# Kernel tuning notes

Measured on AMD Instinct MI355X. Metric: run time of the kernel, lower is better.

The kernel has to match this reference:

```python
import jax, jax.numpy as jnp
import numpy as np
import math

N, S, R = 1, 128, 256
CM, CZ, C, MSA_H, PAIR_H, CTM, FF = 256, 128, 32, 8, 4, 128, 4
SCALE = 1.0 / math.sqrt(C)


def _ln(x, w, b):
    m = jnp.mean(x, -1, keepdims=True)
    v = jnp.var(x, -1, keepdims=True)
    return (x - m) / jnp.sqrt(v + 1e-5) * w + b


def _gated_attn(x, gate_w, qkv_w, out_w, head, bias=None):
    # x: [n, s, r, cin]; attention over r within each (n, s, head)
    n, s, r, _ = x.shape
    gate = jax.nn.sigmoid(x @ gate_w).reshape(n, s, r, head, C)
    qkv = (x @ qkv_w).reshape(n, s, r, 3, head, C)
    q, k, v = qkv[..., 0, :, :], qkv[..., 1, :, :], qkv[..., 2, :, :]
    sim = jax.nn.softmax(jnp.einsum('nsqhc,nskhc->nshqk', q, k) * SCALE, axis=-1)
    if bias is not None:
        sim = sim + bias  # NOTE: source adds bias AFTER softmax; kept faithful
    att = jnp.einsum('nshqk,nskhc->nsqhc', sim, v) * gate
    return att.reshape(n, s, r, head * C) @ out_w


def _tri_mul(x, n1w, n1b, n2w, n2b, p1, p2, p3, p4, p5, p6, incoming):
    xn = _ln(x, n1w, n1b)
    a = jax.nn.sigmoid(xn @ p1) * (xn @ p2)
    b = jax.nn.sigmoid(xn @ p3) * (xn @ p4)
    if incoming:
        p = jnp.einsum('nrsk,nrtk->nstk', a, b)
        g = jnp.swapaxes(jax.nn.sigmoid(xn @ p6), 1, 2)
    else:
        p = jnp.einsum('nsrk,ntrk->nstk', a, b)
        g = jax.nn.sigmoid(xn @ p6)
    return (_ln(p, n2w, n2b) @ p5) * g


def setup_inputs() -> dict:
    keys = iter(jax.random.split(jax.random.key(0), 80))

    def rn(shape, scale=0.02):
        return jax.random.normal(next(keys), shape, dtype=jnp.float32) * scale

    ones = lambda n: jnp.ones((n,), jnp.float32)
    zeros = lambda n: jnp.zeros((n,), jnp.float32)
    d = dict(
        msa_repr=rn((N, S, R, CM), 1.0),
        pair_repr=rn((N, R, R, CZ), 1.0),
        row_norm_m_w=ones(CM), row_norm_m_b=zeros(CM),
        row_norm_z_w=ones(CZ), row_norm_z_b=zeros(CZ),
        row_gate=rn((CM, MSA_H * C)), row_qkv=rn((CM, 3 * MSA_H * C)),
        row_out=rn((MSA_H * C, CM)), row_bias=rn((CZ, MSA_H)),
        col_norm_w=ones(CM), col_norm_b=zeros(CM),
        col_gate=rn((CM, MSA_H * C)), col_qkv=rn((CM, 3 * MSA_H * C)),
        col_out=rn((MSA_H * C, CM)),
        mt_norm_w=ones(CM), mt_norm_b=zeros(CM),
        mt_p1=rn((CM, FF * CM)), mt_p2=rn((FF * CM, CM)),
        outer_norm_w=ones(CM), outer_norm_b=zeros(CM),
        outer_p1=rn((CM, C)), outer_p2=rn((CM, C)), outer_out=rn((C * C, CZ)),
        tmo_n1_w=ones(CZ), tmo_n1_b=zeros(CZ), tmo_n2_w=ones(CTM), tmo_n2_b=zeros(CTM),
        tmo_p1=rn((CZ, CTM)), tmo_p2=rn((CZ, CTM)), tmo_p3=rn((CZ, CTM)), tmo_p4=rn((CZ, CTM)),
        tmo_p5=rn((CTM, CZ)), tmo_p6=rn((CZ, CZ)),
        tmi_n1_w=ones(CZ), tmi_n1_b=zeros(CZ), tmi_n2_w=ones(CTM), tmi_n2_b=zeros(CTM),
        tmi_p1=rn((CZ, CTM)), tmi_p2=rn((CZ, CTM)), tmi_p3=rn((CZ, CTM)), tmi_p4=rn((CZ, CTM)),
        tmi_p5=rn((CTM, CZ)), tmi_p6=rn((CZ, CZ)),
        tas_norm_w=ones(CZ), tas_norm_b=zeros(CZ),
        tas_gate=rn((CZ, PAIR_H * C)), tas_qkv=rn((CZ, 3 * PAIR_H * C)),
        tas_out=rn((PAIR_H * C, CZ)), tas_bias=rn((CZ, PAIR_H)),
        tae_norm_w=ones(CZ), tae_norm_b=zeros(CZ),
        tae_gate=rn((CZ, PAIR_H * C)), tae_qkv=rn((CZ, 3 * PAIR_H * C)),
        tae_out=rn((PAIR_H * C, CZ)), tae_bias=rn((CZ, PAIR_H)),
        pt_norm_w=ones(CZ), pt_norm_b=zeros(CZ),
        pt_p1=rn((CZ, FF * CZ)), pt_p2=rn((FF * CZ, CZ)),
    )
    return d


def reference(msa_repr, pair_repr, row_norm_m_w, row_norm_m_b, row_norm_z_w, row_norm_z_b, row_gate, row_qkv, row_out, row_bias, col_norm_w, col_norm_b, col_gate, col_qkv, col_out, mt_norm_w, mt_norm_b, mt_p1, mt_p2, outer_norm_w, outer_norm_b, outer_p1, outer_p2, outer_out, tmo_n1_w, tmo_n1_b, tmo_n2_w, tmo_n2_b, tmo_p1, tmo_p2, tmo_p3, tmo_p4, tmo_p5, tmo_p6, tmi_n1_w, tmi_n1_b, tmi_n2_w, tmi_n2_b, tmi_p1, tmi_p2, tmi_p3, tmi_p4, tmi_p5, tmi_p6, tas_norm_w, tas_norm_b, tas_gate, tas_qkv, tas_out, tas_bias, tae_norm_w, tae_norm_b, tae_gate, tae_qkv, tae_out, tae_bias, pt_norm_w, pt_norm_b, pt_p1, pt_p2):
    msa, pair = msa_repr, pair_repr
    # 1. MSA row attention with pair bias
    xm = _ln(msa, row_norm_m_w, row_norm_m_b)
    xz = _ln(pair, row_norm_z_w, row_norm_z_b)
    bias = jnp.transpose(xz @ row_bias, (0, 3, 1, 2))[:, None]  # [N,1,H,R,R]
    msa = msa + _gated_attn(xm, row_gate, row_qkv, row_out, MSA_H, bias)
    # 2. MSA column attention
    xm = _ln(msa, col_norm_w, col_norm_b)
    msa = msa + jnp.swapaxes(_gated_attn(jnp.swapaxes(xm, 1, 2), col_gate, col_qkv, col_out, MSA_H), 1, 2)
    # 3. MSA transition
    xm = _ln(msa, mt_norm_w, mt_norm_b)
    msa = msa + jax.nn.relu(xm @ mt_p1) @ mt_p2
    # 4. outer product mean (no division in source; sum over s)
    xm = _ln(msa, outer_norm_w, outer_norm_b)
    a = jnp.swapaxes(xm @ outer_p1, 1, 2)  # [n,r,s,c]
    b = jnp.swapaxes(xm @ outer_p2, 1, 2)  # [n,t,s,c]
    outer = jnp.einsum('nrsc,ntse->nrtce', a, b).reshape(a.shape[0], a.shape[1], b.shape[1], C * C)
    pair = pair + outer @ outer_out
    # 5/6. triangle multiplicative updates (outgoing then incoming)
    pair = pair + _tri_mul(pair, tmo_n1_w, tmo_n1_b, tmo_n2_w, tmo_n2_b, tmo_p1, tmo_p2, tmo_p3, tmo_p4, tmo_p5, tmo_p6, False)
    pair = pair + _tri_mul(pair, tmi_n1_w, tmi_n1_b, tmi_n2_w, tmi_n2_b, tmi_p1, tmi_p2, tmi_p3, tmi_p4, tmi_p5, tmi_p6, True)
    # 7. triangle attention (node start)
    xz = _ln(pair, tas_norm_w, tas_norm_b)
    bias = jnp.transpose(xz @ tas_bias, (0, 1, 3, 2))[:, :, :, None, :]  # [N,S,H,1,R]
    pair = pair + _gated_attn(xz, tas_gate, tas_qkv, tas_out, PAIR_H, bias)
    # 8. triangle attention (node end): transpose residue axes
    xz = jnp.swapaxes(_ln(pair, tae_norm_w, tae_norm_b), 1, 2)
    bias = jnp.transpose(xz @ tae_bias, (0, 1, 3, 2))[:, :, :, None, :]
    pair = pair + jnp.swapaxes(_gated_attn(xz, tae_gate, tae_qkv, tae_out, PAIR_H, bias), 1, 2)
    # 9. pair transition
    xz = _ln(pair, pt_norm_w, pt_norm_b)
    pair = pair + jax.nn.relu(xz @ pt_p1) @ pt_p2
    return msa, pair
```

## Files before the change

kernel.cpp:

```cpp
#include <hip/hip_runtime.h>
#include <hip/hip_bf16.h>
#include <stdint.h>

typedef __hip_bfloat16 bf16;
typedef __attribute__((ext_vector_type(4))) int   i32x4;
typedef __attribute__((ext_vector_type(4))) float f32x4;


__device__ __forceinline__ float toF(float x){ return x; }
__device__ __forceinline__ float toF(bf16 x){ return __bfloat162float(x); }
__device__ __forceinline__ bf16  toB(float x){ return __float2bfloat16(x); }

__device__ __forceinline__ void gload16(const bf16* g, bf16* l){
    __builtin_amdgcn_global_load_lds((const __attribute__((address_space(1))) void*)g,
                                     (__attribute__((address_space(3))) void*)l, 16, 0, 0);
}

__global__ void cvt_w_k(const void* __restrict__ in, bf16* __restrict__ out, int n,
                        const uint32_t* __restrict__ probe){
    bool isbf = (probe[0] == 0x3F803F80u);
    int i = blockIdx.x*256 + threadIdx.x;
    if (i < n) out[i] = isbf ? ((const bf16*)in)[i] : toB(((const float*)in)[i]);
}
__global__ void cvt_wT_k(const void* __restrict__ in, bf16* __restrict__ out, int K, int N,
                         const uint32_t* __restrict__ probe){
    bool isbf = (probe[0] == 0x3F803F80u);
    int i = blockIdx.x*256 + threadIdx.x;
    if (i < K*N){
        float v = isbf ? toF(((const bf16*)in)[i]) : ((const float*)in)[i];
        int k = i / N, n = i - k*N;
        out[(size_t)n*K + k] = toB(v);
    }
}
__global__ void in2f_k(const void* __restrict__ in, float* __restrict__ out, int n,
                       const uint32_t* __restrict__ probe){
    bool isbf = (probe[0] == 0x3F803F80u);
    int i = blockIdx.x*256 + threadIdx.x;
    if (i < n) out[i] = isbf ? toF(((const bf16*)in)[i]) : ((const float*)in)[i];
}

template<typename T>
__global__ void ln_k(const T* __restrict__ x, const bf16* __restrict__ w, const bf16* __restrict__ b,
                     bf16* __restrict__ out, int D){
    int row = blockIdx.x, c = threadIdx.x;
    float v = toF(x[(size_t)row*D + c]);
    float s1 = v, s2 = v*v;
    #pragma unroll
    for (int o=32;o>0;o>>=1){ s1 += __shfl_down(s1,o); s2 += __shfl_down(s2,o); }
    __shared__ float r1[4], r2[4];
    int lane = c & 63, wid = c >> 6;
    if (lane==0){ r1[wid]=s1; r2[wid]=s2; }
    __syncthreads();
    int nw = blockDim.x >> 6;
    float m=0.f, q=0.f;
    for (int i=0;i<nw;i++){ m+=r1[i]; q+=r2[i]; }
    m /= (float)D; q = q/(float)D - m*m;
    float inv = rsqrtf(q + 1e-5f);
    out[(size_t)row*D + c] = toB((v-m)*inv*toF(w[c]) + toF(b[c]));
}

template<int MODE, int HN>
__global__ __launch_bounds__(256) void bproj_k(const bf16* __restrict__ xz, const bf16* __restrict__ Wb,
                                               float* __restrict__ outb){
    __shared__ float WbS[128*HN];
    const int i = blockIdx.x, t = threadIdx.x;
    for (int idx = t; idx < 128*HN; idx += 256) WbS[idx] = toF(Wb[idx]);
    __syncthreads();
    const bf16* row = xz + ((size_t)i*256 + t)*128;
    float d[HN] = {};
    #pragma unroll 4
    for (int c8 = 0; c8 < 16; ++c8){
        uint4 v = *(const uint4*)(row + c8*8);
        bf16 tmp[8]; *(uint4*)tmp = v;
        #pragma unroll
        for (int u=0;u<8;u++){
            float x = toF(tmp[u]);
            #pragma unroll
            for (int h=0;h<HN;h++) d[h] += x * WbS[(c8*8+u)*HN + h];
        }
    }
    #pragma unroll
    for (int h=0;h<HN;h++){
        size_t idx = (MODE==0) ? ((size_t)h*65536 + (size_t)i*256 + t)
                   : (MODE==1) ? ((size_t)(i*HN+h)*256 + t)
                               : ((size_t)(t*HN+h)*256 + i);
        outb[idx] = d[h];
    }
}

template<int ACT, int MUL, int RES>
__global__ __launch_bounds__(256) void mgemm_k(const bf16* __restrict__ A, const bf16* __restrict__ Bt,
                                               bf16* __restrict__ C, float* __restrict__ Res,
                                               const bf16* __restrict__ Mul,
                                               int M, int N, int K, int ldbt, int res_off, int gtrans){
    __shared__ alignas(16) bf16 As[128*32];
    __shared__ alignas(16) bf16 Bs[128*32];
    const int tid  = threadIdx.x;
    const int m0   = blockIdx.y << 7, n0 = blockIdx.x << 7;
    const int lane = tid & 63, w = tid >> 6;
    const int wr   = (w >> 1) << 6, wc = (w & 1) << 6;
    const int fr   = lane & 15, fq = lane >> 4;
    const int sr = tid >> 2, sc = (tid & 3) << 3;
    const bf16* ga = A  + (size_t)(m0 + sr)*K    + sc;
    const bf16* gb = Bt + (size_t)(n0 + sr)*ldbt + sc;
    bf16* la = As + tid*8;
    bf16* lb = Bs + tid*8;
    const size_t gaS = (size_t)64*K, gbS = (size_t)64*ldbt;

    f32x4 acc[4][4] = {};
    for (int k0=0; k0<K; k0+=32){
        gload16(ga, la);        gload16(ga + gaS, la + 2048);
        gload16(gb, lb);        gload16(gb + gbS, lb + 2048);
        ga += 32; gb += 32;
        __syncthreads();
        i32x4 af[4], bv[4];
        #pragma unroll
        for (int i=0;i<4;i++) af[i] = *(const i32x4*)(As + ((wr + i*16 + fr) << 5) + (fq << 3));
        #pragma unroll
        for (int j=0;j<4;j++) bv[j] = *(const i32x4*)(Bs + ((wc + j*16 + fr) << 5) + (fq << 3));
        #pragma unroll
        for (int i=0;i<4;i++)
            #pragma unroll
            for (int j=0;j<4;j++)
                asm("v_mfma_f32_16x16x32_bf16 %0, %1, %2, %0"
                    : "+v"(acc[i][j]) : "v"(af[i]), "v"(bv[j]));
        __syncthreads();
    }
    #pragma unroll
    for (int i=0;i<4;i++){
        const int mB = m0 + wr + i*16 + (fq << 2);
        #pragma unroll
        for (int j=0;j<4;j++){
            const int n = n0 + wc + j*16 + fr;
            #pragma unroll
            for (int r=0;r<4;r++){
                int m = mB + r;
                float x = acc[i][j][r];
                if (ACT==1) x = 1.f/(1.f + __expf(-x));
                else if (ACT==2) x = fmaxf(x, 0.f);
                if (MUL){
                    int mr = gtrans ? (((m & 255) << 8) | (m >> 8)) : m;
                    x *= toF(Mul[(size_t)mr*N + n]);
                }
                if (RES) Res[(size_t)(m + res_off)*N + n] += x;
                else     C[(size_t)m*N + n] = toB(x);
            }
        }
    }
}

__global__ __launch_bounds__(256) void btrimul_k(const bf16* __restrict__ aT, const bf16* __restrict__ bT,
                                                 bf16* __restrict__ pT){
    __shared__ alignas(16) bf16 As[128*32];
    __shared__ alignas(16) bf16 Bs[128*32];
    const int tid  = threadIdx.x;
    const int m0   = blockIdx.y << 7, n0 = blockIdx.x << 7;
    const size_t zb = (size_t)blockIdx.z << 16;
    const int lane = tid & 63, w = tid >> 6;
    const int wr   = (w >> 1) << 6, wc = (w & 1) << 6;
    const int fr   = lane & 15, fq = lane >> 4;
    const int sr = tid >> 2, sc = (tid & 3) << 3;
    const bf16* ga = aT + zb + (size_t)(m0 + sr)*256 + sc;
    const bf16* gb = bT + zb + (size_t)(n0 + sr)*256 + sc;
    bf16* la = As + tid*8;
    bf16* lb = Bs + tid*8;
    const size_t gS = (size_t)64*256;

    f32x4 acc[4][4] = {};
    for (int k0=0; k0<256; k0+=32){
        gload16(ga, la);        gload16(ga + gS, la + 2048);
        gload16(gb, lb);        gload16(gb + gS, lb + 2048);
        ga += 32; gb += 32;
        __syncthreads();
        i32x4 af[4], bv[4];
        #pragma unroll
        for (int i=0;i<4;i++) af[i] = *(const i32x4*)(As + ((wr + i*16 + fr) << 5) + (fq << 3));
        #pragma unroll
        for (int j=0;j<4;j++) bv[j] = *(const i32x4*)(Bs + ((wc + j*16 + fr) << 5) + (fq << 3));
        #pragma unroll
        for (int i=0;i<4;i++)
            #pragma unroll
            for (int j=0;j<4;j++)
                asm("v_mfma_f32_16x16x32_bf16 %0, %1, %2, %0"
                    : "+v"(acc[i][j]) : "v"(af[i]), "v"(bv[j]));
        __syncthreads();
    }
    #pragma unroll
    for (int i=0;i<4;i++){
        const int mB = m0 + wr + i*16 + (fq << 2);
        #pragma unroll
        for (int j=0;j<4;j++){
            const int n = n0 + wc + j*16 + fr;
            #pragma unroll
            for (int r=0;r<4;r++)
                pT[zb + (size_t)(mB + r)*256 + n] = toB(acc[i][j][r]);
        }
    }
}

__global__ __launch_bounds__(256) void rc2k_k(const bf16* __restrict__ in, bf16* __restrict__ out, int swap){
    __shared__ uint16_t T[128][137];
    const int tt = blockIdx.x, tid = threadIdx.x;
    size_t base_pp, out_off; int ppstride;
    if (!swap){ base_pp = (size_t)tt*128;                  ppstride = 1;   out_off = (size_t)tt*128; }
    else      { int J = tt>>1, I0 = (tt&1)*128;
                base_pp = (size_t)I0*256 + J;              ppstride = 256; out_off = (size_t)J*256 + I0; }
    for (int it=0; it<8; ++it){
        int idx = tid + it*256;
        int r = idx >> 4, c8 = (idx & 15) << 3;
        uint4 v = *(const uint4*)(in + (base_pp + (size_t)r*ppstride)*128 + c8);
        uint16_t tmp[8]; *(uint4*)tmp = v;
        #pragma unroll
        for (int t=0;t<8;t++) T[r][c8+t] = tmp[t];
    }
    __syncthreads();
    for (int it=0; it<8; ++it){
        int idx = tid + it*256;
        int k = idx >> 4, r8 = (idx & 15) << 3;
        uint16_t tmp[8];
        #pragma unroll
        for (int t=0;t<8;t++) tmp[t] = T[r8+t][k];
        *(uint4*)(out + (size_t)k*65536 + out_off + r8) = *(uint4*)tmp;
    }
}
__global__ __launch_bounds__(256) void k2rc_k(const bf16* __restrict__ in, bf16* __restrict__ out){
    __shared__ uint16_t T[128][137];
    const int tt = blockIdx.x, tid = threadIdx.x;
    const size_t a0 = (size_t)tt*128;
    for (int it=0; it<8; ++it){
        int idx = tid + it*256;
        int k = idx >> 4, r8 = (idx & 15) << 3;
        uint4 v = *(const uint4*)(in + (size_t)k*65536 + a0 + r8);
        uint16_t tmp[8]; *(uint4*)tmp = v;
        #pragma unroll
        for (int t=0;t<8;t++) T[r8+t][k] = tmp[t];
    }
    __syncthreads();
    for (int it=0; it<8; ++it){
        int idx = tid + it*256;
        int r = idx >> 4, c8 = (idx & 15) << 3;
        uint16_t tmp[8];
        #pragma unroll
        for (int t=0;t<8;t++) tmp[t] = T[r][c8+t];
        *(uint4*)(out + (a0 + r)*128 + c8) = *(uint4*)tmp;
    }
}

template<int ACT, int MUL, int RES>
__global__ __launch_bounds__(256) void gemm_k(const bf16* __restrict__ A, const bf16* __restrict__ Bw,
                                              bf16* __restrict__ C, float* __restrict__ Res,
                                              const bf16* __restrict__ Mul,
                                              int M, int N, int K, int ldb, int res_off, int gtrans){
    __shared__ float As[64][33];
    __shared__ float Bs[32][65];
    int tid = threadIdx.x;
    int m0 = blockIdx.y*64, n0 = blockIdx.x*64;
    int tx = tid & 15, ty = tid >> 4;
    float acc[4][4] = {};
    for (int k0=0; k0<K; k0+=32){
        for (int i=tid; i<64*32; i+=256){
            int r = i>>5, cc = i&31;
            As[r][cc] = toF(A[(size_t)(m0+r)*K + k0 + cc]);
        }
        for (int i=tid; i<32*64; i+=256){
            int r = i>>6, cc = i&63; int col = n0+cc;
            Bs[r][cc] = (col < N) ? toF(Bw[(size_t)(k0+r)*ldb + col]) : 0.f;
        }
        __syncthreads();
        #pragma unroll 8
        for (int k=0;k<32;k++){
            float a4[4], b4[4];
            #pragma unroll
            for (int i=0;i<4;i++) a4[i] = As[ty*4+i][k];
            #pragma unroll
            for (int j=0;j<4;j++) b4[j] = Bs[k][tx*4+j];
            #pragma unroll
            for (int i=0;i<4;i++)
                #pragma unroll
                for (int j=0;j<4;j++) acc[i][j] += a4[i]*b4[j];
        }
        __syncthreads();
    }
    #pragma unroll
    for (int i=0;i<4;i++){
        int m = m0 + ty*4 + i;
        #pragma unroll
        for (int j=0;j<4;j++){
            int n = n0 + tx*4 + j;
            if (n >= N) continue;
            float x = acc[i][j];
            if (ACT==1) x = 1.f/(1.f + __expf(-x));
            else if (ACT==2) x = fmaxf(x, 0.f);
            if (MUL){
                int mr = gtrans ? (((m & 255) << 8) | (m >> 8)) : m;
                x *= toF(Mul[(size_t)mr*N + n]);
            }
            if (RES) Res[(size_t)(m + res_off)*N + n] += x;
            else     C[(size_t)m*N + n] = toB(x);
        }
    }
}

template<int BIAS, int L>
__global__ __launch_bounds__(256) void attn4_k(bf16* __restrict__ QO,
                                               const bf16* __restrict__ Kp, const bf16* __restrict__ Vp,
                                               const float* __restrict__ bias,
                                               int H, int sO, int sL){
    constexpr int MW  = L/4;
    constexpr int IFR = MW/16;
    constexpr int KC  = 32;
    constexpr int NCH = L/KC;
    constexpr int VP  = L + 8;
    __shared__ alignas(16) bf16 K_lds[L*40];
    __shared__ alignas(16) bf16 VT_lds[32*VP];
    __shared__ alignas(16) bf16 P_lds[L*40];
    __shared__ float red[8*32 + 32];
    const int o = blockIdx.y, h = blockIdx.x, tid = threadIdx.x;
    const int GN = H*32;
    const int lane = tid & 63, w = tid >> 6;
    const int fr = lane & 15, fq = lane >> 4;

    for (int idx = tid; idx < L*4; idx += 256){
        int l = idx >> 2, c8 = (idx & 3) << 3;
        size_t p = (size_t)(o*sO + l*sL)*GN + h*32 + c8;
        *(uint4*)(K_lds + l*40 + c8) = *(const uint4*)(Kp + p);
        uint4 vv = *(const uint4*)(Vp + p);
        bf16 tmp[8]; *(uint4*)tmp = vv;
        #pragma unroll
        for (int t=0;t<8;t++) VT_lds[(c8+t)*VP + l] = tmp[t];
    }
    __syncthreads();

    float* ObS = red + 256;
    if (BIAS == 2){
        int c = tid & 31, g = tid >> 5;
        const float* bp = bias + (size_t)(o*H + h)*256;
        float p = 0.f;
        for (int k = g*(L/8); k < (g+1)*(L/8); ++k)
            p += bp[k] * toF(VT_lds[c*VP + k]);
        red[g*32 + c] = p;
        __syncthreads();
        if (tid < 32){
            float s = 0.f;
            #pragma unroll
            for (int g2=0; g2<8; ++g2) s += red[g2*32 + tid];
            ObS[tid] = s;
        }
        __syncthreads();
    }

    i32x4 qf[IFR];
    #pragma unroll
    for (int i=0;i<IFR;i++){
        int q = w*MW + i*16 + fr;
        qf[i] = *(const i32x4*)(QO + (size_t)(o*sO + q*sL)*GN + h*32 + fq*8);
    }
    bf16* Pw = P_lds + w*MW*40;
    f32x4 accO[IFR][2] = {};
    f32x4 accB[IFR][2] = {};
    float lsum[IFR][4] = {};

    for (int ch=0; ch<NCH; ++ch){
        const int k0 = ch*KC;
        f32x4 sa[IFR][2] = {};
        i32x4 kf[2];
        #pragma unroll
        for (int j=0;j<2;j++) kf[j] = *(const i32x4*)(K_lds + (k0 + j*16 + fr)*40 + fq*8);
        #pragma unroll
        for (int i=0;i<IFR;i++)
            #pragma unroll
            for (int j=0;j<2;j++)
                asm("v_mfma_f32_16x16x32_bf16 %0, %1, %2, %0"
                    : "+v"(sa[i][j]) : "v"(qf[i]), "v"(kf[j]));
        #pragma unroll
        for (int i=0;i<IFR;i++)
            #pragma unroll
            for (int j=0;j<2;j++)
                #pragma unroll
                for (int r=0;r<4;r++){
                    float e = __expf(sa[i][j][r] * 0.17677669529663687f);
                    lsum[i][r] += e;
                    Pw[(i*16 + fq*4 + r)*40 + j*16 + fr] = toB(e);
                }
        i32x4 vf[2];
        #pragma unroll
        for (int j=0;j<2;j++) vf[j] = *(const i32x4*)(VT_lds + (j*16 + fr)*VP + k0 + fq*8);
        #pragma unroll
        for (int i=0;i<IFR;i++){
            i32x4 pa = *(const i32x4*)(Pw + (i*16 + fr)*40 + fq*8);
            #pragma unroll
            for (int j=0;j<2;j++)
                asm("v_mfma_f32_16x16x32_bf16 %0, %1, %2, %0"
                    : "+v"(accO[i][j]) : "v"(pa), "v"(vf[j]));
        }
        if (BIAS == 1){
            #pragma unroll
            for (int it=0; it<32; ++it){
                int q = it*2 + (lane>>5), kk = lane&31;
                Pw[q*40 + kk] = toB(bias[(size_t)h*65536 + (size_t)(w*MW + q)*256 + k0 + kk]);
            }
            #pragma unroll
            for (int i=0;i<IFR;i++){
                i32x4 pa = *(const i32x4*)(Pw + (i*16 + fr)*40 + fq*8);
                #pragma unroll
                for (int j=0;j<2;j++)
                    asm("v_mfma_f32_16x16x32_bf16 %0, %1, %2, %0"
                        : "+v"(accB[i][j]) : "v"(pa), "v"(vf[j]));
            }
        }
    }
    #pragma unroll
    for (int i=0;i<IFR;i++)
        #pragma unroll
        for (int r=0;r<4;r++){
            float s = lsum[i][r];
            s += __shfl_xor(s, 1); s += __shfl_xor(s, 2);
            s += __shfl_xor(s, 4); s += __shfl_xor(s, 8);
            lsum[i][r] = 1.f / s;
        }
    #pragma unroll
    for (int i=0;i<IFR;i++)
        #pragma unroll
        for (int j=0;j<2;j++)
            #pragma unroll
            for (int r=0;r<4;r++){
                int q = w*MW + i*16 + fq*4 + r;
                int c = j*16 + fr;
                float v = accO[i][j][r]*lsum[i][r];
                if (BIAS==1) v += accB[i][j][r];
                if (BIAS==2) v += ObS[c];
                QO[(size_t)(o*sO + q*sL)*GN + h*32 + c] = toB(v);
            }
}

__global__ void mulsig_k(bf16* __restrict__ a, const bf16* __restrict__ g, int n){
    int i = blockIdx.x*256 + threadIdx.x;
    if (i < n){
        float sg = 1.f/(1.f + __expf(-toF(g[i])));
        a[i] = toB(toF(a[i]) * sg);
    }
}

__global__ __launch_bounds__(256) void outer_k(const bf16* __restrict__ ap, const bf16* __restrict__ bp,
                                               bf16* __restrict__ outc, int r0){
    int t = blockIdx.x, rl = blockIdx.y, r = r0 + rl;
    __shared__ float As[128*32], Bs[128*32];
    for (int idx=threadIdx.x; idx<128*32; idx+=256){
        int s = idx>>5, c = idx&31;
        As[idx] = toF(ap[((size_t)s*256 + r)*32 + c]);
        Bs[idx] = toF(bp[((size_t)s*256 + t)*32 + c]);
    }
    __syncthreads();
    int ce0 = threadIdx.x*4;
    int c = ce0 >> 5, e0 = ce0 & 31;
    float acc[4] = {0.f,0.f,0.f,0.f};
    for (int s=0;s<128;s++){
        float av = As[s*32 + c];
        #pragma unroll
        for (int j=0;j<4;j++) acc[j] += av*Bs[s*32 + e0 + j];
    }
    size_t row = (size_t)rl*256 + t;
    #pragma unroll
    for (int j=0;j<4;j++) outc[row*1024 + ce0 + j] = toB(acc[j]);
}

static bool tshape(int i, int& K, int& N){
    switch(i){
        case 6: case 8: case 12: case 14: K=256; N=256;  return true;
        case 7: case 13:                  K=256; N=768;  return true;
        case 17:                          K=256; N=1024; return true;
        case 18:                          K=1024;N=256;  return true;
        case 23:                          K=1024;N=128;  return true;
        case 47: case 53:                 K=128; N=384;  return true;
        case 58:                          K=128; N=512;  return true;
        case 59:                          K=512; N=128;  return true;
        default:
            if ((i>=28&&i<=33)||(i>=38&&i<=43)||i==46||i==48||i==52||i==54){ K=128; N=128; return true; }
            return false;
    }
}

extern "C" void kernel_launch(void* const* d_in, const int* in_sizes, int n_in,
                              void* d_out, int out_size, void* d_ws, size_t ws_size,
                              hipStream_t stream){
    (void)n_in; (void)out_size; (void)ws_size;
    const int MSA_N  = 128*256*256;
    const int PAIR_N = 256*256*128;
    const uint32_t* probe = (const uint32_t*)d_in[2];

    char*  w     = (char*)d_ws;
    bf16*  wsts  = (bf16*)(w);
    float* biasF = (float*)(w + 4194304);
    bf16*  lnb   = (bf16*)(w + 6291456);
    bf16*  bufA  = (bf16*)(w + 23068672);
    bf16*  bufB  = (bf16*)(w + 39845888);
    bf16*  bufC  = (bf16*)(w + 56623104);

    float* msaF  = (float*)d_out;
    float* pairF = msaF + MSA_N;

    size_t woff[64]; { size_t acc = 0;
        for (int i=2;i<60;i++){ woff[i] = acc; acc += ((size_t)in_sizes[i] + 63) & ~(size_t)63; } }
    #define W(i) (wsts + woff[i])
    for (int i=2;i<60;i++){
        int tk, tn;
        if (tshape(i, tk, tn))
            cvt_wT_k<<<(in_sizes[i]+255)/256,256,0,stream>>>(d_in[i], W(i), tk, tn, probe);
        else
            cvt_w_k<<<(in_sizes[i]+255)/256,256,0,stream>>>(d_in[i], W(i), in_sizes[i], probe);
    }

    in2f_k<<<32768,256,0,stream>>>(d_in[0], msaF,  MSA_N,  probe);
    in2f_k<<<32768,256,0,stream>>>(d_in[1], pairF, PAIR_N, probe);

    #define GEMM_GRID(M,N) dim3(((N)+63)/64, (M)/64)
    #define MG(M,N)        dim3((N)/128, (M)/128)

    ln_k<float><<<32768,256,0,stream>>>(msaF, W(2), W(3), lnb, 256);
    ln_k<float><<<65536,128,0,stream>>>(pairF, W(4), W(5), bufC, 128);
    bproj_k<0,8><<<256,256,0,stream>>>(bufC, W(9), biasF);
    mgemm_k<0,0,0><<<MG(32768,256),256,0,stream>>>(lnb, W(7),        bufA, nullptr, nullptr, 32768,256,256, 256, 0,0);
    mgemm_k<0,0,0><<<MG(32768,256),256,0,stream>>>(lnb, W(7)+65536,  bufB, nullptr, nullptr, 32768,256,256, 256, 0,0);
    mgemm_k<0,0,0><<<MG(32768,256),256,0,stream>>>(lnb, W(7)+131072, bufC, nullptr, nullptr, 32768,256,256, 256, 0,0);
    attn4_k<1,256><<<dim3(8,128),256,0,stream>>>(bufA, bufB, bufC, biasF, 8, 256, 1);
    mgemm_k<0,0,0><<<MG(32768,256),256,0,stream>>>(lnb, W(6), bufB, nullptr, nullptr, 32768,256,256, 256, 0,0);
    mulsig_k<<<32768,256,0,stream>>>(bufA, bufB, MSA_N);
    mgemm_k<0,0,1><<<MG(32768,256),256,0,stream>>>(bufA, W(8), nullptr, msaF, nullptr, 32768,256,256, 256, 0,0);

    ln_k<float><<<32768,256,0,stream>>>(msaF, W(10), W(11), lnb, 256);
    mgemm_k<0,0,0><<<MG(32768,256),256,0,stream>>>(lnb, W(13),        bufA, nullptr, nullptr, 32768,256,256, 256, 0,0);
    mgemm_k<0,0,0><<<MG(32768,256),256,0,stream>>>(lnb, W(13)+65536,  bufB, nullptr, nullptr, 32768,256,256, 256, 0,0);
    mgemm_k<0,0,0><<<MG(32768,256),256,0,stream>>>(lnb, W(13)+131072, bufC, nullptr, nullptr, 32768,256,256, 256, 0,0);
    attn4_k<0,128><<<dim3(8,256),256,0,stream>>>(bufA, bufB, bufC, nullptr, 8, 1, 256);
    mgemm_k<0,0,0><<<MG(32768,256),256,0,stream>>>(lnb, W(12), bufB, nullptr, nullptr, 32768,256,256, 256, 0,0);
    mulsig_k<<<32768,256,0,stream>>>(bufA, bufB, MSA_N);
    mgemm_k<0,0,1><<<MG(32768,256),256,0,stream>>>(bufA, W(14), nullptr, msaF, nullptr, 32768,256,256, 256, 0,0);

    ln_k<float><<<32768,256,0,stream>>>(msaF, W(15), W(16), lnb, 256);
    for (int ch=0; ch<4; ++ch){
        mgemm_k<2,0,0><<<MG(32768,256),256,0,stream>>>(lnb, W(17)+ch*65536, bufA, nullptr, nullptr, 32768,256,256, 256, 0,0);
        mgemm_k<0,0,1><<<MG(32768,256),256,0,stream>>>(bufA, W(18)+ch*256, nullptr, msaF, nullptr, 32768,256,256, 1024, 0,0);
    }

    ln_k<float><<<32768,256,0,stream>>>(msaF, W(19), W(20), lnb, 256);
    gemm_k<0,0,0><<<GEMM_GRID(32768,32),256,0,stream>>>(lnb, W(21), bufA, nullptr, nullptr, 32768,32,256, 32, 0,0);
    gemm_k<0,0,0><<<GEMM_GRID(32768,32),256,0,stream>>>(lnb, W(22), bufB, nullptr, nullptr, 32768,32,256, 32, 0,0);
    for (int ch=0; ch<8; ++ch){
        outer_k<<<dim3(256,32),256,0,stream>>>(bufA, bufB, lnb, ch*32);
        mgemm_k<0,0,1><<<MG(8192,128),256,0,stream>>>(lnb, W(23), nullptr, pairF, nullptr, 8192,128,1024, 1024, ch*8192,0);
    }

    for (int tm=0; tm<2; ++tm){
        int o = tm ? 34 : 24;
        int inc = tm;
        ln_k<float><<<65536,128,0,stream>>>(pairF, W(o+0), W(o+1), lnb, 128);
        mgemm_k<1,0,0><<<MG(65536,128),256,0,stream>>>(lnb, W(o+4), bufA, nullptr, nullptr, 65536,128,128, 128, 0,0);
        mgemm_k<0,1,0><<<MG(65536,128),256,0,stream>>>(lnb, W(o+5), bufA, nullptr, bufA,   65536,128,128, 128, 0,0);
        mgemm_k<1,0,0><<<MG(65536,128),256,0,stream>>>(lnb, W(o+6), bufB, nullptr, nullptr, 65536,128,128, 128, 0,0);
        mgemm_k<0,1,0><<<MG(65536,128),256,0,stream>>>(lnb, W(o+7), bufB, nullptr, bufB,   65536,128,128, 128, 0,0);
        rc2k_k<<<512,256,0,stream>>>(bufA, bufC, inc);
        rc2k_k<<<512,256,0,stream>>>(bufB, bufA, inc);
        btrimul_k<<<dim3(2,2,128),256,0,stream>>>(bufC, bufA, bufB);
        k2rc_k<<<512,256,0,stream>>>(bufB, bufC);
        ln_k<bf16><<<65536,128,0,stream>>>(bufC, W(o+2), W(o+3), bufC, 128);
        mgemm_k<1,0,0><<<MG(65536,128),256,0,stream>>>(lnb, W(o+9), bufA, nullptr, nullptr, 65536,128,128, 128, 0,0);
        mgemm_k<0,1,1><<<MG(65536,128),256,0,stream>>>(bufC, W(o+8), nullptr, pairF, bufA, 65536,128,128, 128, 0, inc);
    }

    ln_k<float><<<65536,128,0,stream>>>(pairF, W(44), W(45), lnb, 128);
    bproj_k<1,4><<<256,256,0,stream>>>(lnb, W(49), biasF);
    mgemm_k<0,0,0><<<MG(65536,128),256,0,stream>>>(lnb, W(47),       bufA, nullptr, nullptr, 65536,128,128, 128, 0,0);
    mgemm_k<0,0,0><<<MG(65536,128),256,0,stream>>>(lnb, W(47)+16384, bufB, nullptr, nullptr, 65536,128,128, 128, 0,0);
    mgemm_k<0,0,0><<<MG(65536,128),256,0,stream>>>(lnb, W(47)+32768, bufC, nullptr, nullptr, 65536,128,128, 128, 0,0);
    attn4_k<2,256><<<dim3(4,256),256,0,stream>>>(bufA, bufB, bufC, biasF, 4, 256, 1);
    mgemm_k<0,0,0><<<MG(65536,128),256,0,stream>>>(lnb, W(46), bufB, nullptr, nullptr, 65536,128,128, 128, 0,0);
    mulsig_k<<<32768,256,0,stream>>>(bufA, bufB, PAIR_N);
    mgemm_k<0,0,1><<<MG(65536,128),256,0,stream>>>(bufA, W(48), nullptr, pairF, nullptr, 65536,128,128, 128, 0,0);

    ln_k<float><<<65536,128,0,stream>>>(pairF, W(50), W(51), lnb, 128);
    bproj_k<2,4><<<256,256,0,stream>>>(lnb, W(55), biasF);
    mgemm_k<0,0,0><<<MG(65536,128),256,0,stream>>>(lnb, W(53),       bufA, nullptr, nullptr, 65536,128,128, 128, 0,0);
    mgemm_k<0,0,0><<<MG(65536,128),256,0,stream>>>(lnb, W(53)+16384, bufB, nullptr, nullptr, 65536,128,128, 128, 0,0);
    mgemm_k<0,0,0><<<MG(65536,128),256,0,stream>>>(lnb, W(53)+32768, bufC, nullptr, nullptr, 65536,128,128, 128, 0,0);
    attn4_k<2,256><<<dim3(4,256),256,0,stream>>>(bufA, bufB, bufC, biasF, 4, 1, 256);
    mgemm_k<0,0,0><<<MG(65536,128),256,0,stream>>>(lnb, W(52), bufB, nullptr, nullptr, 65536,128,128, 128, 0,0);
    mulsig_k<<<32768,256,0,stream>>>(bufA, bufB, PAIR_N);
    mgemm_k<0,0,1><<<MG(65536,128),256,0,stream>>>(bufA, W(54), nullptr, pairF, nullptr, 65536,128,128, 128, 0,0);

    ln_k<float><<<65536,128,0,stream>>>(pairF, W(56), W(57), lnb, 128);
    for (int ch=0; ch<4; ++ch){
        mgemm_k<2,0,0><<<MG(65536,128),256,0,stream>>>(lnb, W(58)+ch*16384, bufA, nullptr, nullptr, 65536,128,128, 128, 0,0);
        mgemm_k<0,0,1><<<MG(65536,128),256,0,stream>>>(bufA, W(59)+ch*128, nullptr, pairF, nullptr, 65536,128,128, 512, 0,0);
    }
}
```

Baseline: 2.518 ms.

## Fuse QKV projections and add weight-resident skinny GEMM with fused gating

Merges the three separate Q/K/V projection GEMMs into one wide GEMM writing an interleaved buffer, with attention and gating kernels reading it through new leading-dimension strides. Adds an sgemm_k kernel that keeps the full 128x128 weight in swizzled LDS and streams A directly from global memory. For triangle-mult projections it computes sigmoid(x@W1)*(x@W2) in one pass, and the gate GEMM multiplies in the attention output directly, dropping separate launches and the mulsig passes. The intent is to cut launches and intermediate reads and writes. In exchange, sgemm reads A fragments from global memory without LDS staging and uses large LDS per block, which may limit occupancy.

```diff
diff --git a/kernel.cpp b/kernel.cpp
--- a/kernel.cpp
+++ b/kernel.cpp
@@ -92,7 +92,8 @@
 __global__ __launch_bounds__(256) void mgemm_k(const bf16* __restrict__ A, const bf16* __restrict__ Bt,
                                                bf16* __restrict__ C, float* __restrict__ Res,
                                                const bf16* __restrict__ Mul,
-                                               int M, int N, int K, int ldbt, int res_off, int gtrans){
+                                               int M, int N, int K, int lda, int ldbt, int ldc,
+                                               int res_off, int gtrans){
     __shared__ alignas(16) bf16 As[128*32];
     __shared__ alignas(16) bf16 Bs[128*32];
     const int tid  = threadIdx.x;
@@ -101,11 +102,11 @@
     const int wr   = (w >> 1) << 6, wc = (w & 1) << 6;
     const int fr   = lane & 15, fq = lane >> 4;
     const int sr = tid >> 2, sc = (tid & 3) << 3;
-    const bf16* ga = A  + (size_t)(m0 + sr)*K    + sc;
+    const bf16* ga = A  + (size_t)(m0 + sr)*lda  + sc;
     const bf16* gb = Bt + (size_t)(n0 + sr)*ldbt + sc;
     bf16* la = As + tid*8;
     bf16* lb = Bs + tid*8;
-    const size_t gaS = (size_t)64*K, gbS = (size_t)64*ldbt;
+    const size_t gaS = (size_t)64*lda, gbS = (size_t)64*ldbt;
 
     f32x4 acc[4][4] = {};
     for (int k0=0; k0<K; k0+=32){
@@ -143,7 +144,74 @@
                     x *= toF(Mul[(size_t)mr*N + n]);
                 }
                 if (RES) Res[(size_t)(m + res_off)*N + n] += x;
-                else     C[(size_t)m*N + n] = toB(x);
+                else     C[(size_t)m*ldc + n] = toB(x);
+            }
+        }
+    }
+}
+
+template<int ACT, int MUL, int RES, int GATE>
+__global__ __launch_bounds__(256) void sgemm_k(const bf16* __restrict__ A,
+        const bf16* __restrict__ Bt1, const bf16* __restrict__ Bt2,
+        bf16* __restrict__ C, float* __restrict__ Res, const bf16* __restrict__ Mul,
+        int M, int lda, int ldbt, int ldc, int ldmul, int res_off, int gtrans){
+    __shared__ alignas(16) bf16 Bs1[128*128];
+    __shared__ alignas(16) bf16 Bs2[GATE ? 128*128 : 16];
+    const int tid = threadIdx.x;
+    for (int idx = tid; idx < 2048; idx += 256){
+        int n = idx >> 4, cc = idx & 15;
+        int sc = (cc ^ (n & 15)) << 3;
+        *(uint4*)(Bs1 + n*128 + sc) = *(const uint4*)(Bt1 + (size_t)n*ldbt + (cc<<3));
+        if (GATE)
+            *(uint4*)(Bs2 + n*128 + sc) = *(const uint4*)(Bt2 + (size_t)n*ldbt + (cc<<3));
+    }
+    __syncthreads();
+    const int lane = tid & 63, w = tid >> 6;
+    const int fr = lane & 15, fq = lane >> 4;
+    const int mb = blockIdx.x*128 + w*32;
+    f32x4 acc[2][8] = {};
+    f32x4 acc2[2][8] = {};
+    #pragma unroll
+    for (int k0=0;k0<4;k0++){
+        i32x4 af[2];
+        #pragma unroll
+        for (int i=0;i<2;i++)
+            af[i] = *(const i32x4*)(A + (size_t)(mb + i*16 + fr)*lda + k0*32 + fq*8);
+        const int co = ((k0*4 + fq) ^ fr) << 3;
+        #pragma unroll
+        for (int j=0;j<8;j++){
+            i32x4 bf1 = *(const i32x4*)(Bs1 + (j*16+fr)*128 + co);
+            #pragma unroll
+            for (int i=0;i<2;i++)
+                asm("v_mfma_f32_16x16x32_bf16 %0, %1, %2, %0"
+                    : "+v"(acc[i][j]) : "v"(af[i]), "v"(bf1));
+            if (GATE){
+                i32x4 bf2 = *(const i32x4*)(Bs2 + (j*16+fr)*128 + co);
+                #pragma unroll
+                for (int i=0;i<2;i++)
+                    asm("v_mfma_f32_16x16x32_bf16 %0, %1, %2, %0"
+                        : "+v"(acc2[i][j]) : "v"(af[i]), "v"(bf2));
+            }
+        }
+    }
+    #pragma unroll
+    for (int i=0;i<2;i++){
+        #pragma unroll
+        for (int j=0;j<8;j++){
+            const int n = j*16 + fr;
+            #pragma unroll
+            for (int r=0;r<4;r++){
+                int m = mb + i*16 + (fq<<2) + r;
+                float x = acc[i][j][r];
+                if (GATE) x = acc2[i][j][r] / (1.f + __expf(-x));
+                else if (ACT==1) x = 1.f/(1.f + __expf(-x));
+                else if (ACT==2) x = fmaxf(x, 0.f);
+                if (MUL){
+                    int mr = gtrans ? (((m & 255) << 8) | (m >> 8)) : m;
+                    x *= toF(Mul[(size_t)mr*ldmul + n]);
+                }
+                if (RES) Res[(size_t)(m + res_off)*128 + n] += x;
+                else     C[(size_t)m*ldc + n] = toB(x);
             }
         }
     }
@@ -305,7 +373,7 @@
 __global__ __launch_bounds__(256) void attn4_k(bf16* __restrict__ QO,
                                                const bf16* __restrict__ Kp, const bf16* __restrict__ Vp,
                                                const float* __restrict__ bias,
-                                               int H, int sO, int sL){
+                                               int H, int GN, int sO, int sL){
     constexpr int MW  = L/4;
     constexpr int IFR = MW/16;
     constexpr int KC  = 32;
@@ -316,7 +384,6 @@
     __shared__ alignas(16) bf16 P_lds[L*40];
     __shared__ float red[8*32 + 32];
     const int o = blockIdx.y, h = blockIdx.x, tid = threadIdx.x;
-    const int GN = H*32;
     const int lane = tid & 63, w = tid >> 6;
     const int fr = lane & 15, fq = lane >> 4;
 
@@ -433,11 +500,13 @@
             }
 }
 
-__global__ void mulsig_k(bf16* __restrict__ a, const bf16* __restrict__ g, int n){
+__global__ void mulsig2_k(bf16* __restrict__ a, int n){
     int i = blockIdx.x*256 + threadIdx.x;
     if (i < n){
-        float sg = 1.f/(1.f + __expf(-toF(g[i])));
-        a[i] = toB(toF(a[i]) * sg);
+        int m = i >> 8, c = i & 255;
+        size_t o = (size_t)m*768 + c;
+        float sg = 1.f/(1.f + __expf(-toF(a[o + 256])));
+        a[o] = toB(toF(a[o]) * sg);
     }
 }
 
@@ -513,83 +582,88 @@
     in2f_k<<<32768,256,0,stream>>>(d_in[0], msaF,  MSA_N,  probe);
     in2f_k<<<32768,256,0,stream>>>(d_in[1], pairF, PAIR_N, probe);
 
-    #define GEMM_GRID(M,N) dim3(((N)+63)/64, (M)/64)
-    #define MG(M,N)        dim3((N)/128, (M)/128)
-
     ln_k<float><<<32768,256,0,stream>>>(msaF, W(2), W(3), lnb, 256);
     ln_k<float><<<65536,128,0,stream>>>(pairF, W(4), W(5), bufC, 128);
     bproj_k<0,8><<<256,256,0,stream>>>(bufC, W(9), biasF);
-    mgemm_k<0,0,0><<<MG(32768,256),256,0,stream>>>(lnb, W(7),        bufA, nullptr, nullptr, 32768,256,256, 256, 0,0);
-    mgemm_k<0,0,0><<<MG(32768,256),256,0,stream>>>(lnb, W(7)+65536,  bufB, nullptr, nullptr, 32768,256,256, 256, 0,0);
-    mgemm_k<0,0,0><<<MG(32768,256),256,0,stream>>>(lnb, W(7)+131072, bufC, nullptr, nullptr, 32768,256,256, 256, 0,0);
-    attn4_k<1,256><<<dim3(8,128),256,0,stream>>>(bufA, bufB, bufC, biasF, 8, 256, 1);
-    mgemm_k<0,0,0><<<MG(32768,256),256,0,stream>>>(lnb, W(6), bufB, nullptr, nullptr, 32768,256,256, 256, 0,0);
-    mulsig_k<<<32768,256,0,stream>>>(bufA, bufB, MSA_N);
-    mgemm_k<0,0,1><<<MG(32768,256),256,0,stream>>>(bufA, W(8), nullptr, msaF, nullptr, 32768,256,256, 256, 0,0);
+    mgemm_k<0,0,0><<<dim3(6,256),256,0,stream>>>(lnb, W(7), bufA, nullptr, nullptr,
+                                                 32768,768,256, 256,256,768, 0,0);
+    attn4_k<1,256><<<dim3(8,128),256,0,stream>>>(bufA, bufA+256, bufA+512, biasF, 8, 768, 256, 1);
+    mgemm_k<0,0,0><<<dim3(2,256),256,0,stream>>>(lnb, W(6), bufA+256, nullptr, nullptr,
+                                                 32768,256,256, 256,256,768, 0,0);
+    mulsig2_k<<<32768,256,0,stream>>>(bufA, MSA_N);
+    mgemm_k<0,0,1><<<dim3(2,256),256,0,stream>>>(bufA, W(8), nullptr, msaF, nullptr,
+                                                 32768,256,256, 768,256,256, 0,0);
 
     ln_k<float><<<32768,256,0,stream>>>(msaF, W(10), W(11), lnb, 256);
-    mgemm_k<0,0,0><<<MG(32768,256),256,0,stream>>>(lnb, W(13),        bufA, nullptr, nullptr, 32768,256,256, 256, 0,0);
-    mgemm_k<0,0,0><<<MG(32768,256),256,0,stream>>>(lnb, W(13)+65536,  bufB, nullptr, nullptr, 32768,256,256, 256, 0,0);
-    mgemm_k<0,0,0><<<MG(32768,256),256,0,stream>>>(lnb, W(13)+131072, bufC, nullptr, nullptr, 32768,256,256, 256, 0,0);
-    attn4_k<0,128><<<dim3(8,256),256,0,stream>>>(bufA, bufB, bufC, nullptr, 8, 1, 256);
-    mgemm_k<0,0,0><<<MG(32768,256),256,0,stream>>>(lnb, W(12), bufB, nullptr, nullptr, 32768,256,256, 256, 0,0);
-    mulsig_k<<<32768,256,0,stream>>>(bufA, bufB, MSA_N);
-    mgemm_k<0,0,1><<<MG(32768,256),256,0,stream>>>(bufA, W(14), nullptr, msaF, nullptr, 32768,256,256, 256, 0,0);
+    mgemm_k<0,0,0><<<dim3(6,256),256,0,stream>>>(lnb, W(13), bufA, nullptr, nullptr,
+                                                 32768,768,256, 256,256,768, 0,0);
+    attn4_k<0,128><<<dim3(8,256),256,0,stream>>>(bufA, bufA+256, bufA+512, nullptr, 8, 768, 1, 256);
+    mgemm_k<0,0,0><<<dim3(2,256),256,0,stream>>>(lnb, W(12), bufA+256, nullptr, nullptr,
+                                                 32768,256,256, 256,256,768, 0,0);
+    mulsig2_k<<<32768,256,0,stream>>>(bufA, MSA_N);
+    mgemm_k<0,0,1><<<dim3(2,256),256,0,stream>>>(bufA, W(14), nullptr, msaF, nullptr,
+                                                 32768,256,256, 768,256,256, 0,0);
 
     ln_k<float><<<32768,256,0,stream>>>(msaF, W(15), W(16), lnb, 256);
     for (int ch=0; ch<4; ++ch){
-        mgemm_k<2,0,0><<<MG(32768,256),256,0,stream>>>(lnb, W(17)+ch*65536, bufA, nullptr, nullptr, 32768,256,256, 256, 0,0);
-        mgemm_k<0,0,1><<<MG(32768,256),256,0,stream>>>(bufA, W(18)+ch*256, nullptr, msaF, nullptr, 32768,256,256, 1024, 0,0);
+        mgemm_k<2,0,0><<<dim3(2,256),256,0,stream>>>(lnb, W(17)+ch*65536, bufA, nullptr, nullptr,
+                                                     32768,256,256, 256,256,256, 0,0);
+        mgemm_k<0,0,1><<<dim3(2,256),256,0,stream>>>(bufA, W(18)+ch*256, nullptr, msaF, nullptr,
+                                                     32768,256,256, 256,1024,256, 0,0);
     }
 
     ln_k<float><<<32768,256,0,stream>>>(msaF, W(19), W(20), lnb, 256);
-    gemm_k<0,0,0><<<GEMM_GRID(32768,32),256,0,stream>>>(lnb, W(21), bufA, nullptr, nullptr, 32768,32,256, 32, 0,0);
-    gemm_k<0,0,0><<<GEMM_GRID(32768,32),256,0,stream>>>(lnb, W(22), bufB, nullptr, nullptr, 32768,32,256, 32, 0,0);
+    gemm_k<0,0,0><<<dim3(1,512),256,0,stream>>>(lnb, W(21), bufA, nullptr, nullptr, 32768,32,256, 32, 0,0);
+    gemm_k<0,0,0><<<dim3(1,512),256,0,stream>>>(lnb, W(22), bufB, nullptr, nullptr, 32768,32,256, 32, 0,0);
     for (int ch=0; ch<8; ++ch){
         outer_k<<<dim3(256,32),256,0,stream>>>(bufA, bufB, lnb, ch*32);
-        mgemm_k<0,0,1><<<MG(8192,128),256,0,stream>>>(lnb, W(23), nullptr, pairF, nullptr, 8192,128,1024, 1024, ch*8192,0);
+        mgemm_k<0,0,1><<<dim3(1,64),256,0,stream>>>(lnb, W(23), nullptr, pairF, nullptr,
+                                                    8192,128,1024, 1024,1024,128, ch*8192,0);
     }
 
     for (int tm=0; tm<2; ++tm){
         int o = tm ? 34 : 24;
         int inc = tm;
         ln_k<float><<<65536,128,0,stream>>>(pairF, W(o+0), W(o+1), lnb, 128);
-        mgemm_k<1,0,0><<<MG(65536,128),256,0,stream>>>(lnb, W(o+4), bufA, nullptr, nullptr, 65536,128,128, 128, 0,0);
-        mgemm_k<0,1,0><<<MG(65536,128),256,0,stream>>>(lnb, W(o+5), bufA, nullptr, bufA,   65536,128,128, 128, 0,0);
-        mgemm_k<1,0,0><<<MG(65536,128),256,0,stream>>>(lnb, W(o+6), bufB, nullptr, nullptr, 65536,128,128, 128, 0,0);
-        mgemm_k<0,1,0><<<MG(65536,128),256,0,stream>>>(lnb, W(o+7), bufB, nullptr, bufB,   65536,128,128, 128, 0,0);
+        sgemm_k<0,0,0,1><<<512,256,0,stream>>>(lnb, W(o+4), W(o+5), bufA, nullptr, nullptr,
+                                               65536, 128,128,128,0, 0,0);
+        sgemm_k<0,0,0,1><<<512,256,0,stream>>>(lnb, W(o+6), W(o+7), bufB, nullptr, nullptr,
+                                               65536, 128,128,128,0, 0,0);
         rc2k_k<<<512,256,0,stream>>>(bufA, bufC, inc);
         rc2k_k<<<512,256,0,stream>>>(bufB, bufA, inc);
         btrimul_k<<<dim3(2,2,128),256,0,stream>>>(bufC, bufA, bufB);
         k2rc_k<<<512,256,0,stream>>>(bufB, bufC);
         ln_k<bf16><<<65536,128,0,stream>>>(bufC, W(o+2), W(o+3), bufC, 128);
-        mgemm_k<1,0,0><<<MG(65536,128),256,0,stream>>>(lnb, W(o+9), bufA, nullptr, nullptr, 65536,128,128, 128, 0,0);
-        mgemm_k<0,1,1><<<MG(65536,128),256,0,stream>>>(bufC, W(o+8), nullptr, pairF, bufA, 65536,128,128, 128, 0, inc);
+        sgemm_k<1,0,0,0><<<512,256,0,stream>>>(lnb, W(o+9), nullptr, bufA, nullptr, nullptr,
+                                               65536, 128,128,128,0, 0,0);
+        sgemm_k<0,1,1,0><<<512,256,0,stream>>>(bufC, W(o+8), nullptr, nullptr, pairF, bufA,
+                                               65536, 128,128,0,128, 0, inc);
     }
 
     ln_k<float><<<65536,128,0,stream>>>(pairF, W(44), W(45), lnb, 128);
     bproj_k<1,4><<<256,256,0,stream>>>(lnb, W(49), biasF);
-    mgemm_k<0,0,0><<<MG(65536,128),256,0,stream>>>(lnb, W(47),       bufA, nullptr, nullptr, 65536,128,128, 128, 0,0);
-    mgemm_k<0,0,0><<<MG(65536,128),256,0,stream>>>(lnb, W(47)+16384, bufB, nullptr, nullptr, 65536,128,128, 128, 0,0);
-    mgemm_k<0,0,0><<<MG(65536,128),256,0,stream>>>(lnb, W(47)+32768, bufC, nullptr, nullptr, 65536,128,128, 128, 0,0);
-    attn4_k<2,256><<<dim3(4,256),256,0,stream>>>(bufA, bufB, bufC, biasF, 4, 256, 1);
-    mgemm_k<0,0,0><<<MG(65536,128),256,0,stream>>>(lnb, W(46), bufB, nullptr, nullptr, 65536,128,128, 128, 0,0);
-    mulsig_k<<<32768,256,0,stream>>>(bufA, bufB, PAIR_N);
-    mgemm_k<0,0,1><<<MG(65536,128),256,0,stream>>>(bufA, W(48), nullptr, pairF, nullptr, 65536,128,128, 128, 0,0);
-
+    mgemm_k<0,0,0><<<dim3(3,512),256,0,stream>>>(lnb, W(47), bufA, nullptr, nullptr,
+                                                 65536,384,128, 128,128,384, 0,0);
+    attn4_k<2,256><<<dim3(4,256),256,0,stream>>>(bufA, bufA+128, bufA+256, biasF, 4, 384, 256, 1);
+    sgemm_k<1,1,0,0><<<512,256,0,stream>>>(lnb, W(46), nullptr, bufA+128, nullptr, bufA,
+                                           65536, 128,128,384,384, 0,0);
+    sgemm_k<0,0,1,0><<<512,256,0,stream>>>(bufA+128, W(48), nullptr, nullptr, pairF, nullptr,
+                                           65536, 384,128,0,0, 0,0);
     ln_k<float><<<65536,128,0,stream>>>(pairF, W(50), W(51), lnb, 128);
     bproj_k<2,4><<<256,256,0,stream>>>(lnb, W(55), biasF);
-    mgemm_k<0,0,0><<<MG(65536,128),256,0,stream>>>(lnb, W(53),       bufA, nullptr, nullptr, 65536,128,128, 128, 0,0);
-    mgemm_k<0,0,0><<<MG(65536,128),256,0,stream>>>(lnb, W(53)+16384, bufB, nullptr, nullptr, 65536,128,128, 128, 0,0);
-    mgemm_k<0,0,0><<<MG(65536,128),256,0,stream>>>(lnb, W(53)+32768, bufC, nullptr, nullptr, 65536,128,128, 128, 0,0);
-    attn4_k<2,256><<<dim3(4,256),256,0,stream>>>(bufA, bufB, bufC, biasF, 4, 1, 256);
-    mgemm_k<0,0,0><<<MG(65536,128),256,0,stream>>>(lnb, W(52), bufB, nullptr, nullptr, 65536,128,128, 128, 0,0);
-    mulsig_k<<<32768,256,0,stream>>>(bufA, bufB, PAIR_N);
-    mgemm_k<0,0,1><<<MG(65536,128),256,0,stream>>>(bufA, W(54), nullptr, pairF, nullptr, 65536,128,128, 128, 0,0);
+    mgemm_k<0,0,0><<<dim3(3,512),256,0,stream>>>(lnb, W(53), bufA, nullptr, nullptr,
+                                                 65536,384,128, 128,128,384, 0,0);
+    attn4_k<2,256><<<dim3(4,256),256,0,stream>>>(bufA, bufA+128, bufA+256, biasF, 4, 384, 1, 256);
+    sgemm_k<1,1,0,0><<<512,256,0,stream>>>(lnb, W(52), nullptr, bufA+128, nullptr, bufA,
+                                           65536, 128,128,384,384, 0,0);
+    sgemm_k<0,0,1,0><<<512,256,0,stream>>>(bufA+128, W(54), nullptr, nullptr, pairF, nullptr,
+                                           65536, 384,128,0,0, 0,0);
 
     ln_k<float><<<65536,128,0,stream>>>(pairF, W(56), W(57), lnb, 128);
     for (int ch=0; ch<4; ++ch){
-        mgemm_k<2,0,0><<<MG(65536,128),256,0,stream>>>(lnb, W(58)+ch*16384, bufA, nullptr, nullptr, 65536,128,128, 128, 0,0);
-        mgemm_k<0,0,1><<<MG(65536,128),256,0,stream>>>(bufA, W(59)+ch*128, nullptr, pairF, nullptr, 65536,128,128, 512, 0,0);
-    }
-}
+        sgemm_k<2,0,0,0><<<512,256,0,stream>>>(lnb, W(58)+ch*16384, nullptr, bufA, nullptr, nullptr,
+                                               65536, 128,128,128,0, 0,0);
+        sgemm_k<0,0,1,0><<<512,256,0,stream>>>(bufA, W(59)+ch*128, nullptr, nullptr, pairF, nullptr,
+                                               65536, 128,512,0,0, 0,0);
+    }
+}
```

After: 2.557 ms. About the same (+1.5%).
